# Kernel optimization log

Hardware: AMD Instinct MI355X
Metric: run time of the kernel (lower is better)

Reference implementation:

```python
import jax, jax.numpy as jnp
import numpy as np

N = 100_000
E = 3_200_000
F_IN = 512
F_OUT = 256
ALPHA = 0.2      # LeakyReLU negative slope
EPS = 9e-15      # matches torch.Tensor([9e-15]) in the original


def setup_inputs() -> dict:
    key = jax.random.key(0)
    k_x, k_e, k_w, k_a, k_b = jax.random.split(key, 5)
    x = jax.random.normal(k_x, (N, F_IN), dtype=jnp.float32)
    edge = jax.random.randint(k_e, (2, E), 0, N, dtype=jnp.int64)
    # xavier_normal-ish scales
    W = jax.random.normal(k_w, (F_IN, F_OUT), dtype=jnp.float32) * (1.414 * np.sqrt(2.0 / (F_IN + F_OUT)))
    a = jax.random.normal(k_a, (2 * F_OUT,), dtype=jnp.float32) * (1.414 * np.sqrt(2.0 / (1 + 2 * F_OUT)))
    bias = jax.random.normal(k_b, (F_OUT,), dtype=jnp.float32) * (1.414 * np.sqrt(2.0 / (1 + F_OUT)))
    return {"x": x, "edge": edge, "W": W, "a": a, "bias": bias}


def reference(x, edge, W, a, bias):
    src, dst = edge[0], edge[1]
    n = x.shape[0]
    h = x @ W + bias  # [N, F_OUT]
    # a . cat(h[src], h[dst]) == (h @ a_src)[src] + (h @ a_dst)[dst]
    a_src, a_dst = a[:F_OUT], a[F_OUT:]
    e = (h @ a_src)[src] + (h @ a_dst)[dst]            # [E]
    e = jnp.where(e > 0, e, ALPHA * e)                  # LeakyReLU
    e = jnp.exp(e - jnp.max(e))                         # global-max stabilized exp
    rowsum = jax.ops.segment_sum(e, src, num_segments=n)               # [N]
    h_prime = jax.ops.segment_sum(e[:, None] * h[dst], src, num_segments=n)  # [N, F_OUT]
    h_prime = h_prime / (rowsum[:, None] + EPS)
    return jax.nn.elu(h_prime)
```

## Files before the change

### kernel.cpp

```cpp
#include <hip/hip_runtime.h>

typedef __bf16 bf16x8 __attribute__((ext_vector_type(8)));
typedef float f32x4 __attribute__((ext_vector_type(4)));
typedef unsigned short u16x8 __attribute__((ext_vector_type(8)));

#define FIN 512
#define FOUT 256
#define NBLK 256
#define BSHIFT 8

__device__ __forceinline__ float b2f(unsigned short u) {
  union { unsigned int u; float f; } x;
  x.u = ((unsigned int)u) << 16;
  return x.f;
}
__device__ __forceinline__ unsigned short f2b(float f) {
  union { float f; unsigned int u; } x; x.f = f;
  unsigned int u = x.u;
  unsigned int r = (u + 0x7fffu + ((u >> 16) & 1u)) >> 16;
  return (unsigned short)r;
}

__global__ void k_probe(const unsigned short* __restrict__ xh,
                        const int* __restrict__ e, int* __restrict__ flags) {
  __shared__ int cnt[2];
  if (threadIdx.x == 0) { cnt[0] = 0; cnt[1] = 0; }
  __syncthreads();
  int c = 0;
  for (int i = threadIdx.x; i < 32768; i += 256) {
    unsigned short u = xh[i];
    if (((u >> 7) & 0xFF) == 0xFF) c++;
  }
  if (c) atomicAdd(&cnt[0], c);
  if (e[2 * threadIdx.x + 1] == 0) atomicAdd(&cnt[1], 1);
  __syncthreads();
  if (threadIdx.x == 0) {
    flags[0] = (cnt[0] > 0) ? 1 : 0;
    flags[1] = (cnt[1] > 128) ? 1 : 0;
  }
}

__global__ void k_transpose(const void* __restrict__ W,
                            unsigned short* __restrict__ Wt,
                            const int* __restrict__ flags) {
  int idx = blockIdx.x * 256 + threadIdx.x;
  int k = idx >> 8, n = idx & 255;
  float v = flags[0] ? ((const float*)W)[idx]
                     : b2f(((const unsigned short*)W)[idx]);
  Wt[n * FIN + k] = f2b(v);
}

__global__ __launch_bounds__(256) void k_gemm(const void* __restrict__ X,
                                              const unsigned short* __restrict__ Wt,
                                              const void* __restrict__ bias,
                                              unsigned short* __restrict__ H,
                                              int nrows, const int* __restrict__ flags) {
  __shared__ char lds[65536];
  const int tid = threadIdx.x;
  const int wave = tid >> 6;
  const int lane = tid & 63;
  const int fm = lane & 15;
  const int fq = lane >> 4;
  const int isf = flags[0];
  const int m0 = blockIdx.x * 64;

  if (isf) {
#pragma unroll 4
    for (int j = 0; j < 16; ++j) {
      int r = wave * 16 + j;
      int grow = m0 + r; if (grow >= nrows) grow = nrows - 1;
      int c = lane ^ (j & 7);
      const float* gp = (const float*)X + (size_t)grow * FIN + c * 8;
      f32x4 lo = *(const f32x4*)gp;
      f32x4 hi = *(const f32x4*)(gp + 4);
      union { bf16x8 v; unsigned short u[8]; } cv;
#pragma unroll
      for (int k = 0; k < 4; k++) { cv.u[k] = f2b(lo[k]); cv.u[4 + k] = f2b(hi[k]); }
      *(bf16x8*)(lds + r * 1024 + lane * 16) = cv.v;
    }
  } else {
#pragma unroll
    for (int j = 0; j < 16; ++j) {
      int r = wave * 16 + j;
      int grow = m0 + r; if (grow >= nrows) grow = nrows - 1;
      int c = lane ^ (j & 7);
      const unsigned short* gp = (const unsigned short*)X + (size_t)grow * FIN + c * 8;
      __builtin_amdgcn_global_load_lds(
          (const __attribute__((address_space(1))) void*)gp,
          (__attribute__((address_space(3))) void*)(lds + r * 1024), 16, 0, 0);
    }
  }
  __syncthreads();

  f32x4 acc[4][4];
#pragma unroll
  for (int i = 0; i < 4; i++)
#pragma unroll
    for (int j = 0; j < 4; j++) acc[i][j] = (f32x4){0.f, 0.f, 0.f, 0.f};

  const unsigned short* wp[4];
#pragma unroll
  for (int i = 0; i < 4; i++)
    wp[i] = Wt + (size_t)((wave * 4 + i) * 16 + fm) * FIN + fq * 8;

  const int swz = fm & 7;
  bf16x8 bcur[4];
#pragma unroll
  for (int i = 0; i < 4; i++) bcur[i] = *(const bf16x8*)(wp[i]);

  for (int it = 0; it < 16; ++it) {
    int itn = (it + 1 < 16) ? it + 1 : 15;
    bf16x8 bnext[4];
#pragma unroll
    for (int i = 0; i < 4; i++) bnext[i] = *(const bf16x8*)(wp[i] + itn * 32);
    bf16x8 af[4];
#pragma unroll
    for (int mt = 0; mt < 4; mt++) {
      int slot = (it * 4 + fq) ^ swz;
      af[mt] = *(const bf16x8*)(lds + (mt * 16 + fm) * 1024 + slot * 16);
    }
#pragma unroll
    for (int mt = 0; mt < 4; mt++)
#pragma unroll
      for (int i = 0; i < 4; i++)
        acc[mt][i] = __builtin_amdgcn_mfma_f32_16x16x32_bf16(af[mt], bcur[i], acc[mt][i], 0, 0, 0);
#pragma unroll
    for (int i = 0; i < 4; i++) bcur[i] = bnext[i];
  }

#pragma unroll
  for (int i = 0; i < 4; i++) {
    int col = (wave * 4 + i) * 16 + fm;
    float bv = isf ? ((const float*)bias)[col] : b2f(((const unsigned short*)bias)[col]);
#pragma unroll
    for (int mt = 0; mt < 4; mt++) {
#pragma unroll
      for (int r = 0; r < 4; r++) {
        int row = m0 + mt * 16 + fq * 4 + r;
        if (row < nrows) H[(size_t)row * FOUT + col] = f2b(acc[mt][i][r] + bv);
      }
    }
  }
}

__global__ __launch_bounds__(256) void k_scores(const unsigned short* __restrict__ H,
                                                const void* __restrict__ a,
                                                float* __restrict__ s1, float* __restrict__ s2,
                                                int n, const int* __restrict__ flags) {
  int wave = threadIdx.x >> 6, lane = threadIdx.x & 63;
  int row = blockIdx.x * 4 + wave;
  if (row >= n) return;
  const ushort4* hp = (const ushort4*)(H + (size_t)row * FOUT);
  ushort4 hv = hp[lane];
  float as0, as1, as2, as3, ad0, ad1, ad2, ad3;
  if (flags[0]) {
    const float* af = (const float*)a;
    f32x4 s = *(const f32x4*)(af + lane * 4);
    f32x4 d = *(const f32x4*)(af + FOUT + lane * 4);
    as0 = s[0]; as1 = s[1]; as2 = s[2]; as3 = s[3];
    ad0 = d[0]; ad1 = d[1]; ad2 = d[2]; ad3 = d[3];
  } else {
    const ushort4* ap = (const ushort4*)a;
    ushort4 s = ap[lane], d = ap[64 + lane];
    as0 = b2f(s.x); as1 = b2f(s.y); as2 = b2f(s.z); as3 = b2f(s.w);
    ad0 = b2f(d.x); ad1 = b2f(d.y); ad2 = b2f(d.z); ad3 = b2f(d.w);
  }
  float h0 = b2f(hv.x), h1 = b2f(hv.y), h2 = b2f(hv.z), h3 = b2f(hv.w);
  float p1 = h0 * as0 + h1 * as1 + h2 * as2 + h3 * as3;
  float p2 = h0 * ad0 + h1 * ad1 + h2 * ad2 + h3 * ad3;
#pragma unroll
  for (int off = 32; off >= 1; off >>= 1) {
    p1 += __shfl_down(p1, off, 64);
    p2 += __shfl_down(p2, off, 64);
  }
  if (lane == 0) { s1[row] = p1; s2[row] = p2; }
}


__global__ __launch_bounds__(256) void k_bcount(const int* __restrict__ e, int E, int chunk,
                                                int nbuck, int* __restrict__ C,
                                                const int* __restrict__ flags) {
  __shared__ int hist[512];
  int t = threadIdx.x, blk = blockIdx.x;
  for (int i = t; i < nbuck; i += 256) hist[i] = 0;
  __syncthreads();
  int lo = blk * chunk, hi = min(E, lo + chunk);
  bool i64 = flags[1] != 0;
  for (int i = lo + t; i < hi; i += 256) {
    int s = i64 ? ((const int2*)e)[i].x : e[i];
    atomicAdd(&hist[s >> BSHIFT], 1);
  }
  __syncthreads();
  for (int i = t; i < nbuck; i += 256) C[blk * nbuck + i] = hist[i];
}

__global__ __launch_bounds__(256) void k_bscanA(const int* __restrict__ C, int nbuck,
                                                int* __restrict__ O, int* __restrict__ btot) {
  int b = blockIdx.x, t = threadIdx.x;
  int lane = t & 63, w = t >> 6;
  int v = C[t * nbuck + b];
  int x = v;
#pragma unroll
  for (int off = 1; off < 64; off <<= 1) {
    int y = __shfl_up(x, off, 64);
    if (lane >= off) x += y;
  }
  __shared__ int ws[4];
  if (lane == 63) ws[w] = x;
  __syncthreads();
  int wbase = (w > 0 ? ws[0] : 0) + (w > 1 ? ws[1] : 0) + (w > 2 ? ws[2] : 0);
  O[t * nbuck + b] = x + wbase - v;
  if (t == 255) btot[b] = x + wbase;
}

__global__ __launch_bounds__(512) void k_bscanB(const int* __restrict__ btot, int nbuck,
                                                int* __restrict__ bbase,
                                                int* __restrict__ rowptr, int N) {
  __shared__ int sh[512];
  int t = threadIdx.x;
  int v = (t < nbuck) ? btot[t] : 0;
  sh[t] = v;
  __syncthreads();
  for (int off = 1; off < 512; off <<= 1) {
    int u = (t >= off) ? sh[t - off] : 0;
    __syncthreads();
    sh[t] += u;
    __syncthreads();
  }
  if (t < nbuck) bbase[t] = sh[t] - v;
  if (t == nbuck - 1) { bbase[nbuck] = sh[t]; rowptr[N] = sh[t]; }
}

__global__ __launch_bounds__(256) void k_bscatter(const int* __restrict__ e, int E, int chunk,
                                                  int nbuck, const int* __restrict__ O,
                                                  const int* __restrict__ bbase,
                                                  int2* __restrict__ stage,
                                                  const int* __restrict__ flags) {
  __shared__ int cur[512];
  int t = threadIdx.x, blk = blockIdx.x;
  for (int i = t; i < nbuck; i += 256) cur[i] = bbase[i] + O[blk * nbuck + i];
  __syncthreads();
  int lo = blk * chunk, hi = min(E, lo + chunk);
  bool i64 = flags[1] != 0;
  for (int i = lo + t; i < hi; i += 256) {
    int s, d;
    if (i64) { s = ((const int2*)e)[i].x; d = ((const int2*)e)[(size_t)E + i].x; }
    else     { s = e[i];                  d = e[E + i]; }
    int pos = atomicAdd(&cur[s >> BSHIFT], 1);
    stage[pos] = make_int2(s, d);
  }
}

__global__ __launch_bounds__(256) void k_fine(const int2* __restrict__ stage,
                                              const int* __restrict__ bbase,
                                              int* __restrict__ rowptr,
                                              int* __restrict__ csrd, int N) {
  __shared__ int hist[256];
  __shared__ int cursor[256];
  __shared__ int ws[4];
  int b = blockIdx.x, t = threadIdx.x;
  int s0 = b << BSHIFT;
  int base = bbase[b], end = bbase[b + 1], cnt = end - base;
  hist[t] = 0;
  __syncthreads();
  for (int i = t; i < cnt; i += 256) atomicAdd(&hist[stage[base + i].x - s0], 1);
  __syncthreads();
  int v = hist[t];
  int lane = t & 63, w = t >> 6;
  int x = v;
#pragma unroll
  for (int off = 1; off < 64; off <<= 1) {
    int y = __shfl_up(x, off, 64);
    if (lane >= off) x += y;
  }
  if (lane == 63) ws[w] = x;
  __syncthreads();
  int wbase = (w > 0 ? ws[0] : 0) + (w > 1 ? ws[1] : 0) + (w > 2 ? ws[2] : 0);
  int excl = x + wbase - v;
  cursor[t] = base + excl;
  if (s0 + t < N) rowptr[s0 + t] = base + excl;
  __syncthreads();
  for (int i = t; i < cnt; i += 256) {
    int2 p = stage[base + i];
    int pos = atomicAdd(&cursor[p.x - s0], 1);
    csrd[pos] = p.y;
  }
}

__global__ __launch_bounds__(256) void k_gather(const unsigned short* __restrict__ H,
                                                const float* __restrict__ s1,
                                                const float* __restrict__ s2,
                                                const int* __restrict__ rowptr,
                                                const int* __restrict__ csrd,
                                                void* __restrict__ out, int n,
                                                const int* __restrict__ flags) {
  int wave = threadIdx.x >> 6, lane = threadIdx.x & 63;
  int row = blockIdx.x * 4 + wave;
  if (row >= n) return;
  int half = lane >> 5;
  int hl = lane & 31;
  int beg = rowptr[row], end = rowptr[row + 1];
  float s1v = s1[row];
  float ac[8];
#pragma unroll
  for (int k = 0; k < 8; k++) ac[k] = 0.f;
  float wsum = 0.f;

#pragma unroll 4
  for (int e = beg; e < end; e += 2) {
    int ei = e + half;
    int ee = (ei < end) ? ei : beg;
    int d = csrd[ee];
    float v = s1v + s2[d];
    v = v > 0.f ? v : 0.2f * v;
    float w = __expf(v);
    if (ei >= end) w = 0.f;
    union { u16x8 v; unsigned short u[8]; } hv;
    hv.v = *(const u16x8*)(H + (size_t)d * FOUT + hl * 8);
    wsum += w;
#pragma unroll
    for (int k = 0; k < 8; k++) ac[k] += w * b2f(hv.u[k]);
  }

#pragma unroll
  for (int k = 0; k < 8; k++) ac[k] += __shfl_down(ac[k], 32, 64);
  wsum += __shfl_down(wsum, 32, 64);

  if (half == 0) {
    float inv = 1.f / (wsum + 9e-15f);
    float o[8];
#pragma unroll
    for (int k = 0; k < 8; k++) {
      float x = ac[k] * inv;
      o[k] = x > 0.f ? x : __expf(x) - 1.f;
    }
    if (flags[0]) {
      float* op = (float*)out + (size_t)row * FOUT + hl * 8;
      *(f32x4*)op = (f32x4){o[0], o[1], o[2], o[3]};
      *(f32x4*)(op + 4) = (f32x4){o[4], o[5], o[6], o[7]};
    } else {
      union { u16x8 v; unsigned short u[8]; } ov;
#pragma unroll
      for (int k = 0; k < 8; k++) ov.u[k] = f2b(o[k]);
      *(u16x8*)((unsigned short*)out + (size_t)row * FOUT + hl * 8) = ov.v;
    }
  }
}

extern "C" void kernel_launch(void* const* d_in, const int* in_sizes, int n_in,
                              void* d_out, int out_size, void* d_ws, size_t ws_size,
                              hipStream_t stream) {
  const void* X = d_in[0];
  const int* edge = (const int*)d_in[1];
  const void* W = d_in[2];
  const void* A = d_in[3];
  const void* B = d_in[4];
  int N_ = in_sizes[0] / FIN;
  int E_ = in_sizes[1] / 2;
  int nbuck = (N_ + 255) >> BSHIFT;
  int chunk = (E_ + NBLK - 1) / NBLK;

  char* p = (char*)d_ws;
  auto alloc = [&](size_t bytes) {
    char* r = p; p += (bytes + 255) & ~(size_t)255; return r;
  };
  int* flags = (int*)alloc(256);
  unsigned short* H  = (unsigned short*)alloc((size_t)N_ * FOUT * 2);
  unsigned short* Wt = (unsigned short*)alloc((size_t)FIN * FOUT * 2);
  float* s1   = (float*)alloc((size_t)N_ * 4);
  float* s2   = (float*)alloc((size_t)N_ * 4);
  int* rowptr = (int*)alloc((size_t)(N_ + 1) * 4);
  int* csrd   = (int*)alloc((size_t)E_ * 4);
  int* C      = (int*)alloc((size_t)NBLK * nbuck * 4);
  int* O      = (int*)alloc((size_t)NBLK * nbuck * 4);
  int* btot   = (int*)alloc((size_t)nbuck * 4);
  int* bbase  = (int*)alloc((size_t)(nbuck + 1) * 4);
  int2* stage = (int2*)alloc((size_t)E_ * 8);

  k_probe<<<1, 256, 0, stream>>>((const unsigned short*)X, edge, flags);
  k_transpose<<<(FIN * FOUT) / 256, 256, 0, stream>>>(W, Wt, flags);
  k_gemm<<<(N_ + 63) / 64, 256, 0, stream>>>(X, Wt, B, H, N_, flags);
  k_scores<<<(N_ + 3) / 4, 256, 0, stream>>>(H, A, s1, s2, N_, flags);
  k_bcount<<<NBLK, 256, 0, stream>>>(edge, E_, chunk, nbuck, C, flags);
  k_bscanA<<<nbuck, 256, 0, stream>>>(C, nbuck, O, btot);
  k_bscanB<<<1, 512, 0, stream>>>(btot, nbuck, bbase, rowptr, N_);
  k_bscatter<<<NBLK, 256, 0, stream>>>(edge, E_, chunk, nbuck, O, bbase, stage, flags);
  k_fine<<<nbuck, 256, 0, stream>>>(stage, bbase, rowptr, csrd, N_);
  k_gather<<<(N_ + 3) / 4, 256, 0, stream>>>(H, s1, s2, rowptr, csrd,
                                             d_out, N_, flags);
}
```

Before: 773.1 us.

## Pack staged edges into one int and prefetch edge scores per wave

The bucket-scatter staging buffer now stores each edge as a single 32-bit word, holding the source's low 8 bits shifted by 17 with the 17-bit destination. This halves the staging traffic in the scatter and fine-sort kernels. The gather kernel also loads up to 64 neighbor indices and their s2 scores cooperatively per wave into shared memory, then walks them from LDS. That removes the dependent csrd-then-s2 global load chain from the inner loop. The packing assumes N fits in 17 bits (N=100000 does), and the LDS staging adds no explicit barrier within the wave.

```diff
diff --git a/kernel.cpp b/kernel.cpp
--- a/kernel.cpp
+++ b/kernel.cpp
@@ -234,7 +234,7 @@
 __global__ __launch_bounds__(256) void k_bscatter(const int* __restrict__ e, int E, int chunk,
                                                   int nbuck, const int* __restrict__ O,
                                                   const int* __restrict__ bbase,
-                                                  int2* __restrict__ stage,
+                                                  int* __restrict__ stage,
                                                   const int* __restrict__ flags) {
   __shared__ int cur[512];
   int t = threadIdx.x, blk = blockIdx.x;
@@ -247,11 +247,11 @@
     if (i64) { s = ((const int2*)e)[i].x; d = ((const int2*)e)[(size_t)E + i].x; }
     else     { s = e[i];                  d = e[E + i]; }
     int pos = atomicAdd(&cur[s >> BSHIFT], 1);
-    stage[pos] = make_int2(s, d);
-  }
-}
-
-__global__ __launch_bounds__(256) void k_fine(const int2* __restrict__ stage,
+    stage[pos] = ((s & 255) << 17) | d;
+  }
+}
+
+__global__ __launch_bounds__(256) void k_fine(const int* __restrict__ stage,
                                               const int* __restrict__ bbase,
                                               int* __restrict__ rowptr,
                                               int* __restrict__ csrd, int N) {
@@ -263,7 +263,7 @@
   int base = bbase[b], end = bbase[b + 1], cnt = end - base;
   hist[t] = 0;
   __syncthreads();
-  for (int i = t; i < cnt; i += 256) atomicAdd(&hist[stage[base + i].x - s0], 1);
+  for (int i = t; i < cnt; i += 256) atomicAdd(&hist[stage[base + i] >> 17], 1);
   __syncthreads();
   int v = hist[t];
   int lane = t & 63, w = t >> 6;
@@ -281,9 +281,9 @@
   if (s0 + t < N) rowptr[s0 + t] = base + excl;
   __syncthreads();
   for (int i = t; i < cnt; i += 256) {
-    int2 p = stage[base + i];
-    int pos = atomicAdd(&cursor[p.x - s0], 1);
-    csrd[pos] = p.y;
+    int p = stage[base + i];
+    int pos = atomicAdd(&cursor[p >> 17], 1);
+    csrd[pos] = p & 0x1FFFF;
   }
 }
 
@@ -294,6 +294,7 @@
                                                 const int* __restrict__ csrd,
                                                 void* __restrict__ out, int n,
                                                 const int* __restrict__ flags) {
+  __shared__ int2 eds[4][64];
   int wave = threadIdx.x >> 6, lane = threadIdx.x & 63;
   int row = blockIdx.x * 4 + wave;
   if (row >= n) return;
@@ -301,25 +302,33 @@
   int hl = lane & 31;
   int beg = rowptr[row], end = rowptr[row + 1];
   float s1v = s1[row];
+  const unsigned short* Hb = H + hl * 8;
   float ac[8];
 #pragma unroll
   for (int k = 0; k < 8; k++) ac[k] = 0.f;
   float wsum = 0.f;
 
+  for (int base = beg; base < end; base += 64) {
+    int cnt = end - base; if (cnt > 64) cnt = 64;
+    int d_pre = 0;
+    float s_pre = -1e30f;
+    if (lane < cnt) { d_pre = csrd[base + lane]; s_pre = s2[d_pre]; }
+    eds[wave][lane] = make_int2(d_pre, __float_as_int(s_pre));
+
 #pragma unroll 4
-  for (int e = beg; e < end; e += 2) {
-    int ei = e + half;
-    int ee = (ei < end) ? ei : beg;
-    int d = csrd[ee];
-    float v = s1v + s2[d];
-    v = v > 0.f ? v : 0.2f * v;
-    float w = __expf(v);
-    if (ei >= end) w = 0.f;
-    union { u16x8 v; unsigned short u[8]; } hv;
-    hv.v = *(const u16x8*)(H + (size_t)d * FOUT + hl * 8);
-    wsum += w;
-#pragma unroll
-    for (int k = 0; k < 8; k++) ac[k] += w * b2f(hv.u[k]);
+    for (int j = 0; j < cnt; j += 2) {
+      int jj = j + half;
+      int2 p = eds[wave][jj];
+      int dd = p.x;
+      float v = s1v + __int_as_float(p.y);
+      v = v > 0.f ? v : 0.2f * v;
+      float w = (jj < cnt) ? __expf(v) : 0.f;
+      union { u16x8 v; unsigned short u[8]; } hv;
+      hv.v = *(const u16x8*)(Hb + (size_t)dd * FOUT);
+      wsum += w;
+#pragma unroll
+      for (int k = 0; k < 8; k++) ac[k] += w * b2f(hv.u[k]);
+    }
   }
 
 #pragma unroll
@@ -375,7 +384,7 @@
   int* O      = (int*)alloc((size_t)NBLK * nbuck * 4);
   int* btot   = (int*)alloc((size_t)nbuck * 4);
   int* bbase  = (int*)alloc((size_t)(nbuck + 1) * 4);
-  int2* stage = (int2*)alloc((size_t)E_ * 8);
+  int* stage  = (int*)alloc((size_t)E_ * 4);
 
   k_probe<<<1, 256, 0, stream>>>((const unsigned short*)X, edge, flags);
   k_transpose<<<(FIN * FOUT) / 256, 256, 0, stream>>>(W, Wt, flags);
```

After: 752.0 us. -2.7%, faster.
